# Kernel optimization log

Measured on AMD Instinct MI355X. Metric: run time of the kernel, lower is better.

The kernel has to match this reference:

```python
import jax, jax.numpy as jnp
import numpy as np

N_HEAD = 16

def setup_inputs() -> dict:
    key = jax.random.key(0)
    ks = jax.random.split(key, 4)
    B, S, D = 2, 2048, 2048
    return {
        "hidden_states": jax.random.normal(ks[0], (B, S, D), dtype=jnp.float32),
        "attention_mask": jnp.ones((B, S), dtype=jnp.float32),
        "W_attn": jax.random.normal(ks[1], (D, 3 * D), dtype=jnp.float32) * (D ** -0.5),
        "b_attn": jnp.zeros((3 * D,), dtype=jnp.float32),
        "W_proj": jax.random.normal(ks[2], (D, D), dtype=jnp.float32) * (D ** -0.5),
        "b_proj": jnp.zeros((D,), dtype=jnp.float32),
        "lambda_param": jnp.float32(0.8),
    }

def reference(hidden_states, attention_mask, W_attn, b_attn, W_proj, b_proj, lambda_param):
    B, S, D = hidden_states.shape
    H = N_HEAD
    hd = D // H          # full head dim (used by V and for the scale)
    qd = hd // 2         # q/k per-head dim after the dual chunk
    scale = hd ** -0.5

    qkv = hidden_states @ W_attn + b_attn            # [B,S,3D]
    q, k, v = jnp.split(qkv, 3, axis=-1)
    q1, q2 = jnp.split(q, 2, axis=-1)                # each [B,S,D/2]
    k1, k2 = jnp.split(k, 2, axis=-1)

    def heads(x, d):  # [B,S,H*d] -> [B,H,S,d]
        return x.reshape(B, S, H, d).transpose(0, 2, 1, 3)

    q1, q2 = heads(q1, qd), heads(q2, qd)
    k1, k2 = heads(k1, qd), heads(k2, qd)
    v = heads(v, hd)

    # additive mask: (1 - m) * -10000, broadcast over heads and query dim
    mask = (1.0 - attention_mask)[:, None, None, :] * -10000.0  # [B,1,1,S]

    s1 = jnp.einsum("bhqd,bhkd->bhqk", q1, k1) * scale + mask
    s2 = jnp.einsum("bhqd,bhkd->bhqk", q2, k2) * scale + mask
    w = jax.nn.softmax(s1, axis=-1) - lambda_param * jax.nn.softmax(s2, axis=-1)

    out = jnp.einsum("bhqk,bhkd->bhqd", w, v)        # [B,H,S,hd]
    out = out.transpose(0, 2, 1, 3).reshape(B, S, D)
    return out @ W_proj + b_proj
```

## Files before the change

kernel.cpp:

```cpp
#include <hip/hip_runtime.h>
#include <hip/hip_bf16.h>

typedef __attribute__((ext_vector_type(8))) short bf16x8;
typedef __attribute__((ext_vector_type(8))) unsigned short u16x8;
typedef __attribute__((ext_vector_type(4))) float f32x4;

__device__ __forceinline__ unsigned short f2bf(float f) {
  union { float f; unsigned int i; } v; v.f = f;
  unsigned int r = v.i + 0x7FFFu + ((v.i >> 16) & 1u);
  return (unsigned short)(r >> 16);
}
__device__ __forceinline__ unsigned int pack2bf_rn(float a, float b) {
  union { float f; unsigned int i; } x, y; x.f = a; y.f = b;
  return ((x.i + 0x8000u) >> 16) | ((y.i + 0x8000u) & 0xFFFF0000u);
}
__device__ __forceinline__ unsigned int cvtpk(float a, float b) {
  unsigned int r;
  asm("v_cvt_pk_bf16_f32 %0, %1, %2" : "=v"(r) : "v"(a), "v"(b));
  return r;
}
__device__ __forceinline__ float fexp2(float x) {
  float r;
  asm("v_exp_f32 %0, %1" : "=v"(r) : "v"(x));
  return r;
}
__device__ __forceinline__ void gll16(const unsigned short* g, unsigned short* l) {
  __builtin_amdgcn_global_load_lds(
      (const __attribute__((address_space(1))) unsigned int*)g,
      (__attribute__((address_space(3))) unsigned int*)l, 16, 0, 0);
}

__device__ __forceinline__ void transpose32(const float* in, unsigned short* out,
                                            long in_rs, long out_rs, int c0, int r0,
                                            unsigned short (*tile)[33]) {
  int tx = threadIdx.x & 31, ty = threadIdx.x >> 5;
#pragma unroll
  for (int i = 0; i < 32; i += 8)
    tile[ty + i][tx] = f2bf(in[(long)(r0 + ty + i) * in_rs + c0 + tx]);
  __syncthreads();
#pragma unroll
  for (int i = 0; i < 32; i += 8)
    out[(long)(c0 + ty + i) * out_rs + r0 + tx] = tile[tx][ty + i];
}

__global__ void prep_k(const float* __restrict__ hs, unsigned short* __restrict__ hsb,
                       const float* __restrict__ Wa, unsigned short* __restrict__ WtA,
                       const float* __restrict__ Wp, unsigned short* __restrict__ WtP) {
  __shared__ unsigned short tile[32][33];
  const int bid = blockIdx.x;
  if (bid < 4096) {
    long i = ((long)bid * 256 + threadIdx.x) * 8;
    float4 a = *(const float4*)(hs + i);
    float4 b = *(const float4*)(hs + i + 4);
    u16x8 o;
    o[0] = f2bf(a.x); o[1] = f2bf(a.y); o[2] = f2bf(a.z); o[3] = f2bf(a.w);
    o[4] = f2bf(b.x); o[5] = f2bf(b.y); o[6] = f2bf(b.z); o[7] = f2bf(b.w);
    *(u16x8*)(hsb + i) = o;
  } else if (bid < 16384) {
    int r = bid - 4096;
    int bx = r % 192, by = r / 192;
    transpose32(Wa, WtA, 6144, 2048, bx * 32, by * 32, tile);
  } else {
    int r = bid - 16384;
    int bx = r & 63, by = r >> 6;
    transpose32(Wp, WtP, 2048, 2048, bx * 32, by * 32, tile);
  }
}


__global__ __launch_bounds__(256) void gemm_qkv(
    const unsigned short* __restrict__ A,
    const unsigned short* __restrict__ Bt,
    const float* __restrict__ bias,
    unsigned short* __restrict__ qQ,
    unsigned short* __restrict__ k1p, unsigned short* __restrict__ k2p,
    unsigned short* __restrict__ vp) {
  const int K = 2048;
  __shared__ unsigned short As[128 * 64];
  __shared__ unsigned short Bs[128 * 64];
  const int m0 = blockIdx.y * 128, n0 = blockIdx.x * 128;
  const int tid = threadIdx.x, lane = tid & 63, wave = tid >> 6;
  const int wm = (wave >> 1) * 64, wn = (wave & 1) * 64;
  const int quad = lane >> 4, l15 = lane & 15;
  const int sw = l15 & 7;
  const int arow = wave * 8 + (lane >> 3);
  const int acol = ((lane & 7) ^ ((lane >> 3) & 7)) * 8;

  f32x4 acc[4][4] = {};
  const unsigned short* Ap = A + (long)(m0 + arow) * K + acol;
  const unsigned short* Bp = Bt + (long)(n0 + arow) * K + acol;
  unsigned short* AsW = As + wave * 512;
  unsigned short* BsW = Bs + wave * 512;

  for (int kb = 0; kb < K; kb += 64) {
    __syncthreads();
#pragma unroll
    for (int s = 0; s < 4; s++) {
      gll16(Ap + s * 32 * K + kb, AsW + s * 2048);
      gll16(Bp + s * 32 * K + kb, BsW + s * 2048);
    }
    __syncthreads();
#pragma unroll
    for (int ks = 0; ks < 2; ks++) {
      bf16x8 af[4], bfr[4];
#pragma unroll
      for (int t = 0; t < 4; t++)
        af[t] = *(const bf16x8*)&As[(wm + t * 16 + l15) * 64 + (((ks * 4 + quad) ^ sw) << 3)];
#pragma unroll
      for (int t = 0; t < 4; t++)
        bfr[t] = *(const bf16x8*)&Bs[(wn + t * 16 + l15) * 64 + (((ks * 4 + quad) ^ sw) << 3)];
#pragma unroll
      for (int i = 0; i < 4; i++)
#pragma unroll
        for (int j = 0; j < 4; j++)
          acc[i][j] = __builtin_amdgcn_mfma_f32_16x16x32_bf16(af[i], bfr[j], acc[i][j], 0, 0, 0);
    }
  }

  const int ncol = n0 + wn;
  if (ncol < 2048) {
#pragma unroll
    for (int j = 0; j < 4; j++) {
      int n = ncol + j * 16 + l15;
      float bv = bias[n];
#pragma unroll
      for (int i = 0; i < 4; i++) {
        int mr = m0 + wm + i * 16 + quad * 4;
#pragma unroll
        for (int r = 0; r < 4; r++)
          qQ[(long)(mr + r) * 2048 + n] = f2bf(acc[i][j][r] + bv);
      }
    }
  } else if (ncol < 4096) {
    unsigned short* kp = (ncol >= 3072) ? k2p : k1p;
#pragma unroll
    for (int j = 0; j < 4; j++) {
      int n = ncol + j * 16 + l15;
      float bv = bias[n];
      int kk = (n - 2048) & 1023;
      int h = kk >> 6, c = (kk >> 3) & 7, e = kk & 7;
#pragma unroll
      for (int i = 0; i < 4; i++) {
        int mr = m0 + wm + i * 16 + quad * 4;
        int b = mr >> 11, s = mr & 2047;
        long tb2 = ((long)(b * 16 + h) * 32 + (s >> 6)) * 4096 + e;
        int row0 = s & 63;
#pragma unroll
        for (int r = 0; r < 4; r++) {
          int row = row0 + r;
          kp[tb2 + row * 64 + ((c ^ (row & 7)) << 3)] = f2bf(acc[i][j][r] + bv);
        }
      }
    }
  } else {
#pragma unroll
    for (int j = 0; j < 4; j++) {
      int n = ncol + j * 16 + l15;
      float bv = bias[n];
      int vv = n - 4096;
      int h = vv >> 7, d = vv & 127;
#pragma unroll
      for (int i = 0; i < 4; i++) {
        int mr = m0 + wm + i * 16 + quad * 4;
        int b = mr >> 11, s = mr & 2047;
        int cc = (s & 63) >> 3;
        long dst = ((long)(b * 16 + h) * 32 + (s >> 6)) * 8192 + d * 64 +
                   ((cc ^ (d & 7)) << 3) + (quad & 1) * 4;
        uint2 st;
        st.x = pack2bf_rn(acc[i][j][0] + bv, acc[i][j][1] + bv);
        st.y = pack2bf_rn(acc[i][j][2] + bv, acc[i][j][3] + bv);
        *(uint2*)&vp[dst] = st;
      }
    }
  }
}

__global__ __launch_bounds__(256) void gemm_bt_f32(
    const unsigned short* __restrict__ A,
    const unsigned short* __restrict__ Bt,
    const float* __restrict__ bias,
    float* __restrict__ C, int K, int ldc) {
  __shared__ unsigned short As[128 * 64];
  __shared__ unsigned short Bs[128 * 64];
  const int m0 = blockIdx.y * 128, n0 = blockIdx.x * 128;
  const int tid = threadIdx.x, lane = tid & 63, wave = tid >> 6;
  const int wm = (wave >> 1) * 64, wn = (wave & 1) * 64;
  const int quad = lane >> 4, l15 = lane & 15;
  const int sw = l15 & 7;
  const int arow = wave * 8 + (lane >> 3);
  const int acol = ((lane & 7) ^ ((lane >> 3) & 7)) * 8;

  f32x4 acc[4][4] = {};
  const unsigned short* Ap = A + (long)(m0 + arow) * K + acol;
  const unsigned short* Bp = Bt + (long)(n0 + arow) * K + acol;
  unsigned short* AsW = As + wave * 512;
  unsigned short* BsW = Bs + wave * 512;

  for (int kb = 0; kb < K; kb += 64) {
    __syncthreads();
#pragma unroll
    for (int s = 0; s < 4; s++) {
      gll16(Ap + (long)s * 32 * K + kb, AsW + s * 2048);
      gll16(Bp + (long)s * 32 * K + kb, BsW + s * 2048);
    }
    __syncthreads();
#pragma unroll
    for (int ks = 0; ks < 2; ks++) {
      bf16x8 af[4], bfr[4];
#pragma unroll
      for (int t = 0; t < 4; t++)
        af[t] = *(const bf16x8*)&As[(wm + t * 16 + l15) * 64 + (((ks * 4 + quad) ^ sw) << 3)];
#pragma unroll
      for (int t = 0; t < 4; t++)
        bfr[t] = *(const bf16x8*)&Bs[(wn + t * 16 + l15) * 64 + (((ks * 4 + quad) ^ sw) << 3)];
#pragma unroll
      for (int i = 0; i < 4; i++)
#pragma unroll
        for (int j = 0; j < 4; j++)
          acc[i][j] = __builtin_amdgcn_mfma_f32_16x16x32_bf16(af[i], bfr[j], acc[i][j], 0, 0, 0);
    }
  }
#pragma unroll
  for (int j = 0; j < 4; j++) {
    int n = n0 + wn + j * 16 + l15;
    float bv = bias[n];
#pragma unroll
    for (int i = 0; i < 4; i++) {
      int mr = m0 + wm + i * 16 + quad * 4;
#pragma unroll
      for (int r = 0; r < 4; r++)
        C[(long)(mr + r) * ldc + n] = acc[i][j][r] + bv;
    }
  }
}

__global__ __launch_bounds__(256, 2) void attn_k(
    const unsigned short* __restrict__ qQ,
    const unsigned short* __restrict__ k1p,
    const unsigned short* __restrict__ k2p,
    const unsigned short* __restrict__ vp,
    const float* __restrict__ mask,
    const float* __restrict__ lamp,
    unsigned short* __restrict__ out) {
  __shared__ unsigned short k1s[2 * 4096];
  __shared__ unsigned short k2s[2 * 4096];
  __shared__ unsigned short vts[2 * 8192];
  __shared__ unsigned short pls[4 * 2048];
  const int bid = blockIdx.x;
  const int wgid = (bid & 7) * 64 + (bid >> 3);
  const int bh = wgid >> 4;
  const int q0 = (wgid & 15) * 128;
  const int b = bh >> 4, h = bh & 15;
  const int tid = threadIdx.x, lane = tid & 63, wave = tid >> 6;
  const int quad = lane >> 4, l15 = lane & 15;
  const long rowq = (long)b * 2048 + q0;
  const int sw = l15 & 7;

  bf16x8 aq1[2][2], aq2[2][2];
#pragma unroll
  for (int qt = 0; qt < 2; qt++) {
    const unsigned short* qr =
        qQ + (rowq + wave * 32 + qt * 16 + l15) * 2048 + h * 64 + quad * 8;
    aq1[qt][0] = *(const bf16x8*)qr;
    aq1[qt][1] = *(const bf16x8*)(qr + 32);
    aq2[qt][0] = *(const bf16x8*)(qr + 1024);
    aq2[qt][1] = *(const bf16x8*)(qr + 1056);
  }
  f32x4 o1[2][8] = {}, o2[2][8] = {};
  f32x4 l1a[2] = {}, l2a[2] = {};
  bf16x8 ones;
#pragma unroll
  for (int e = 0; e < 8; e++) ones[e] = (short)0x3F80;
  const float SL = 0.08838834764831845f * 1.4426950408889634f;
  const float ML = 1.4426950408889634e4f;
  const long tb = (long)bh * 32;
  unsigned short* pw = pls + wave * 2048;

  {
    const unsigned short* k1t = k1p + tb * 4096 + tid * 8;
    const unsigned short* k2t = k2p + tb * 4096 + tid * 8;
    const unsigned short* vtt = vp + tb * 8192 + tid * 8;
    gll16(k1t, k1s + wave * 512);
    gll16(k1t + 2048, k1s + 2048 + wave * 512);
    gll16(k2t, k2s + wave * 512);
    gll16(k2t + 2048, k2s + 2048 + wave * 512);
#pragma unroll
    for (int rr = 0; rr < 4; rr++)
      gll16(vtt + rr * 2048, vts + rr * 2048 + wave * 512);
  }

  for (int t = 0; t < 32; t++) {
    const int cb = t & 1;
    __syncthreads();
    float4 mq[4];
#pragma unroll
    for (int nt = 0; nt < 4; nt++)
      mq[nt] = *(const float4*)(mask + (long)b * 2048 + t * 64 + nt * 16 + quad * 4);
    if (t < 31) {
      const unsigned short* k1t = k1p + (tb + t + 1) * 4096 + tid * 8;
      const unsigned short* k2t = k2p + (tb + t + 1) * 4096 + tid * 8;
      const unsigned short* vtt = vp + (tb + t + 1) * 8192 + tid * 8;
      unsigned short* d1 = k1s + (cb ^ 1) * 4096 + wave * 512;
      unsigned short* d2 = k2s + (cb ^ 1) * 4096 + wave * 512;
      unsigned short* dv = vts + (cb ^ 1) * 8192 + wave * 512;
      gll16(k1t, d1);
      gll16(k1t + 2048, d1 + 2048);
      gll16(k2t, d2);
      gll16(k2t + 2048, d2 + 2048);
#pragma unroll
      for (int rr = 0; rr < 4; rr++)
        gll16(vtt + rr * 2048, dv + rr * 2048);
    }

#pragma unroll
    for (int half = 0; half < 2; half++) {
      f32x4 s1[2][2] = {}, s2[2][2] = {};
#pragma unroll
      for (int np = 0; np < 2; np++) {
        const int row = cb * 4096 + (half * 32 + np * 16 + l15) * 64;
#pragma unroll
        for (int ks = 0; ks < 2; ks++) {
          const int p = ((ks * 4 + quad) ^ sw) * 8;
          bf16x8 kf1 = *(const bf16x8*)&k1s[row + p];
          bf16x8 kf2 = *(const bf16x8*)&k2s[row + p];
#pragma unroll
          for (int qt = 0; qt < 2; qt++) {
            s1[qt][np] = __builtin_amdgcn_mfma_f32_16x16x32_bf16(kf1, aq1[qt][ks], s1[qt][np], 0, 0, 0);
            s2[qt][np] = __builtin_amdgcn_mfma_f32_16x16x32_bf16(kf2, aq2[qt][ks], s2[qt][np], 0, 0, 0);
          }
        }
      }
      float ma[2][4];
#pragma unroll
      for (int np = 0; np < 2; np++)
#pragma unroll
        for (int r = 0; r < 4; r++)
          ma[np][r] = fmaf(((const float*)&mq[half * 2 + np])[r], ML, -ML);
#pragma unroll
      for (int qt = 0; qt < 2; qt++)
#pragma unroll
        for (int np = 0; np < 2; np++) {
          const int addr = l15 * 32 + (((np * 4 + quad) ^ sw) << 2);
          uint2 w1, w2;
          w1.x = cvtpk(fexp2(fmaf(s1[qt][np][0], SL, ma[np][0])),
                       fexp2(fmaf(s1[qt][np][1], SL, ma[np][1])));
          w1.y = cvtpk(fexp2(fmaf(s1[qt][np][2], SL, ma[np][2])),
                       fexp2(fmaf(s1[qt][np][3], SL, ma[np][3])));
          w2.x = cvtpk(fexp2(fmaf(s2[qt][np][0], SL, ma[np][0])),
                       fexp2(fmaf(s2[qt][np][1], SL, ma[np][1])));
          w2.y = cvtpk(fexp2(fmaf(s2[qt][np][2], SL, ma[np][2])),
                       fexp2(fmaf(s2[qt][np][3], SL, ma[np][3])));
          *(uint2*)&pw[(qt * 2 + 0) * 512 + addr] = w1;
          *(uint2*)&pw[(qt * 2 + 1) * 512 + addr] = w2;
        }
      bf16x8 f1[2], f2[2];
      {
        const int ra = l15 * 32 + (((quad * 2 + 0) ^ sw) << 2);
        const int rb = l15 * 32 + (((quad * 2 + 1) ^ sw) << 2);
#pragma unroll
        for (int qt = 0; qt < 2; qt++) {
          union { bf16x8 v; uint2 u2[2]; } g1, g2;
          g1.u2[0] = *(const uint2*)&pw[(qt * 2 + 0) * 512 + ra];
          g1.u2[1] = *(const uint2*)&pw[(qt * 2 + 0) * 512 + rb];
          g2.u2[0] = *(const uint2*)&pw[(qt * 2 + 1) * 512 + ra];
          g2.u2[1] = *(const uint2*)&pw[(qt * 2 + 1) * 512 + rb];
          f1[qt] = g1.v; f2[qt] = g2.v;
        }
      }
#pragma unroll
      for (int qt = 0; qt < 2; qt++) {
        l1a[qt] = __builtin_amdgcn_mfma_f32_16x16x32_bf16(ones, f1[qt], l1a[qt], 0, 0, 0);
        l2a[qt] = __builtin_amdgcn_mfma_f32_16x16x32_bf16(ones, f2[qt], l2a[qt], 0, 0, 0);
      }
#pragma unroll
      for (int dn = 0; dn < 8; dn++) {
        const int pp = ((half * 4 + quad) ^ sw) * 8;
        bf16x8 vf = *(const bf16x8*)&vts[cb * 8192 + (dn * 16 + l15) * 64 + pp];
#pragma unroll
        for (int qt = 0; qt < 2; qt++) {
          o1[qt][dn] = __builtin_amdgcn_mfma_f32_16x16x32_bf16(vf, f1[qt], o1[qt][dn], 0, 0, 0);
          o2[qt][dn] = __builtin_amdgcn_mfma_f32_16x16x32_bf16(vf, f2[qt], o2[qt][dn], 0, 0, 0);
        }
      }
    }
  }
  float lam = lamp[0];
#pragma unroll
  for (int qt = 0; qt < 2; qt++) {
    float i1 = 1.f / l1a[qt][0], i2 = lam / l2a[qt][0];
    unsigned short* orow =
        out + (rowq + wave * 32 + qt * 16 + l15) * 2048 + h * 128 + quad * 4;
#pragma unroll
    for (int dn = 0; dn < 8; dn++) {
      uint2 st;
      st.x = cvtpk(o1[qt][dn][0] * i1 - o2[qt][dn][0] * i2,
                   o1[qt][dn][1] * i1 - o2[qt][dn][1] * i2);
      st.y = cvtpk(o1[qt][dn][2] * i1 - o2[qt][dn][2] * i2,
                   o1[qt][dn][3] * i1 - o2[qt][dn][3] * i2);
      *(uint2*)(orow + dn * 16) = st;
    }
  }
}

extern "C" void kernel_launch(void* const* d_in, const int* in_sizes, int n_in,
                              void* d_out, int out_size, void* d_ws, size_t ws_size,
                              hipStream_t stream) {
  (void)in_sizes; (void)n_in; (void)out_size; (void)ws_size;
  const float* hs   = (const float*)d_in[0];
  const float* mask = (const float*)d_in[1];
  const float* Wa   = (const float*)d_in[2];
  const float* ba   = (const float*)d_in[3];
  const float* Wp   = (const float*)d_in[4];
  const float* bp   = (const float*)d_in[5];
  const float* lam  = (const float*)d_in[6];
  float* out = (float*)d_out;
  unsigned short* ws = (unsigned short*)d_ws;

  unsigned short* hsb = ws;
  unsigned short* WtA = hsb + (long)4096 * 2048;
  unsigned short* WtP = WtA + (long)6144 * 2048;
  unsigned short* qQ  = WtP + (long)2048 * 2048;
  unsigned short* K1p = qQ + (long)4096 * 2048;
  unsigned short* K2p = K1p + (long)2 * 16 * 2048 * 64;
  unsigned short* Vp  = K2p + (long)2 * 16 * 2048 * 64;
  unsigned short* att = hsb;

  prep_k<<<20480, 256, 0, stream>>>(hs, hsb, Wa, WtA, Wp, WtP);
  gemm_qkv<<<dim3(48, 32), 256, 0, stream>>>(hsb, WtA, ba, qQ, K1p, K2p, Vp);
  attn_k<<<512, 256, 0, stream>>>(qQ, K1p, K2p, Vp, mask, lam, att);
  gemm_bt_f32<<<dim3(16, 32), 256, 0, stream>>>(att, WtP, bp, out, 2048, 2048);
}
```

Baseline: 401.2 us.

## Double-buffer LDS tiles in both GEMM kernels to overlap loads with MFMA

Both bf16 GEMM kernels (the QKV projection and the output projection) now keep two LDS buffers for the A and B tiles. The first K-tile is preloaded before the loop, and each iteration issues the global-to-LDS loads for the next tile while the MFMAs run on the current one. This removes one barrier per iteration and is meant to hide global load latency behind compute. In exchange, LDS use per block doubles to 64 KB, which may reduce the number of resident blocks per CU.

```diff
diff --git a/kernel.cpp b/kernel.cpp
--- a/kernel.cpp
+++ b/kernel.cpp
@@ -76,8 +76,8 @@
     unsigned short* __restrict__ k1p, unsigned short* __restrict__ k2p,
     unsigned short* __restrict__ vp) {
   const int K = 2048;
-  __shared__ unsigned short As[128 * 64];
-  __shared__ unsigned short Bs[128 * 64];
+  __shared__ unsigned short As[2 * 128 * 64];
+  __shared__ unsigned short Bs[2 * 128 * 64];
   const int m0 = blockIdx.y * 128, n0 = blockIdx.x * 128;
   const int tid = threadIdx.x, lane = tid & 63, wave = tid >> 6;
   const int wm = (wave >> 1) * 64, wn = (wave & 1) * 64;
@@ -92,23 +92,35 @@
   unsigned short* AsW = As + wave * 512;
   unsigned short* BsW = Bs + wave * 512;
 
+#pragma unroll
+  for (int s = 0; s < 4; s++) {
+    gll16(Ap + (long)s * 32 * K, AsW + s * 2048);
+    gll16(Bp + (long)s * 32 * K, BsW + s * 2048);
+  }
+
   for (int kb = 0; kb < K; kb += 64) {
+    const int cur = (kb >> 6) & 1;
     __syncthreads();
-#pragma unroll
-    for (int s = 0; s < 4; s++) {
-      gll16(Ap + s * 32 * K + kb, AsW + s * 2048);
-      gll16(Bp + s * 32 * K + kb, BsW + s * 2048);
-    }
-    __syncthreads();
+    if (kb + 64 < K) {
+      unsigned short* dA = AsW + (cur ^ 1) * 8192;
+      unsigned short* dB = BsW + (cur ^ 1) * 8192;
+#pragma unroll
+      for (int s = 0; s < 4; s++) {
+        gll16(Ap + (long)s * 32 * K + kb + 64, dA + s * 2048);
+        gll16(Bp + (long)s * 32 * K + kb + 64, dB + s * 2048);
+      }
+    }
+    const unsigned short* Ab = As + cur * 8192;
+    const unsigned short* Bb = Bs + cur * 8192;
 #pragma unroll
     for (int ks = 0; ks < 2; ks++) {
       bf16x8 af[4], bfr[4];
 #pragma unroll
       for (int t = 0; t < 4; t++)
-        af[t] = *(const bf16x8*)&As[(wm + t * 16 + l15) * 64 + (((ks * 4 + quad) ^ sw) << 3)];
+        af[t] = *(const bf16x8*)&Ab[(wm + t * 16 + l15) * 64 + (((ks * 4 + quad) ^ sw) << 3)];
 #pragma unroll
       for (int t = 0; t < 4; t++)
-        bfr[t] = *(const bf16x8*)&Bs[(wn + t * 16 + l15) * 64 + (((ks * 4 + quad) ^ sw) << 3)];
+        bfr[t] = *(const bf16x8*)&Bb[(wn + t * 16 + l15) * 64 + (((ks * 4 + quad) ^ sw) << 3)];
 #pragma unroll
       for (int i = 0; i < 4; i++)
 #pragma unroll
@@ -180,8 +192,8 @@
     const unsigned short* __restrict__ Bt,
     const float* __restrict__ bias,
     float* __restrict__ C, int K, int ldc) {
-  __shared__ unsigned short As[128 * 64];
-  __shared__ unsigned short Bs[128 * 64];
+  __shared__ unsigned short As[2 * 128 * 64];
+  __shared__ unsigned short Bs[2 * 128 * 64];
   const int m0 = blockIdx.y * 128, n0 = blockIdx.x * 128;
   const int tid = threadIdx.x, lane = tid & 63, wave = tid >> 6;
   const int wm = (wave >> 1) * 64, wn = (wave & 1) * 64;
@@ -196,23 +208,35 @@
   unsigned short* AsW = As + wave * 512;
   unsigned short* BsW = Bs + wave * 512;
 
+#pragma unroll
+  for (int s = 0; s < 4; s++) {
+    gll16(Ap + (long)s * 32 * K, AsW + s * 2048);
+    gll16(Bp + (long)s * 32 * K, BsW + s * 2048);
+  }
+
   for (int kb = 0; kb < K; kb += 64) {
+    const int cur = (kb >> 6) & 1;
     __syncthreads();
-#pragma unroll
-    for (int s = 0; s < 4; s++) {
-      gll16(Ap + (long)s * 32 * K + kb, AsW + s * 2048);
-      gll16(Bp + (long)s * 32 * K + kb, BsW + s * 2048);
-    }
-    __syncthreads();
+    if (kb + 64 < K) {
+      unsigned short* dA = AsW + (cur ^ 1) * 8192;
+      unsigned short* dB = BsW + (cur ^ 1) * 8192;
+#pragma unroll
+      for (int s = 0; s < 4; s++) {
+        gll16(Ap + (long)s * 32 * K + kb + 64, dA + s * 2048);
+        gll16(Bp + (long)s * 32 * K + kb + 64, dB + s * 2048);
+      }
+    }
+    const unsigned short* Ab = As + cur * 8192;
+    const unsigned short* Bb = Bs + cur * 8192;
 #pragma unroll
     for (int ks = 0; ks < 2; ks++) {
       bf16x8 af[4], bfr[4];
 #pragma unroll
       for (int t = 0; t < 4; t++)
-        af[t] = *(const bf16x8*)&As[(wm + t * 16 + l15) * 64 + (((ks * 4 + quad) ^ sw) << 3)];
+        af[t] = *(const bf16x8*)&Ab[(wm + t * 16 + l15) * 64 + (((ks * 4 + quad) ^ sw) << 3)];
 #pragma unroll
       for (int t = 0; t < 4; t++)
-        bfr[t] = *(const bf16x8*)&Bs[(wn + t * 16 + l15) * 64 + (((ks * 4 + quad) ^ sw) << 3)];
+        bfr[t] = *(const bf16x8*)&Bb[(wn + t * 16 + l15) * 64 + (((ks * 4 + quad) ^ sw) << 3)];
 #pragma unroll
       for (int i = 0; i < 4; i++)
 #pragma unroll
```

Measured after the change: 411.1 us. +2.5%, slower.
